# Kernel optimization log

Hardware: AMD Instinct MI355X
Metric: run time of the kernel (lower is better)

## Reference

```python
import jax, jax.numpy as jnp
import numpy as np

NEG_SLOPE = 0.2  # PyG GATv2Conv default negative_slope
EPS = 1e-16      # PyG softmax denominator eps


def _gatv2_conv(x, src, dst, Wl, bl, Wr, br, att, bias, heads, out_ch):
    """PyG GATv2Conv (share_weights=False, concat=True, self-loops already in edges)."""
    N = x.shape[0]
    xl = (x @ Wl + bl).reshape(N, heads, out_ch)  # values / source transform
    xr = (x @ Wr + br).reshape(N, heads, out_ch)  # target transform
    m = jax.nn.leaky_relu(xl[src] + xr[dst], NEG_SLOPE)      # [E,H,C]
    e = jnp.einsum('ehc,hc->eh', m, att)                      # [E,H]
    emax = jax.ops.segment_max(e, dst, num_segments=N)       # [N,H]
    ee = jnp.exp(e - emax[dst])
    denom = jax.ops.segment_sum(ee, dst, num_segments=N)
    alpha = ee / (denom[dst] + EPS)                           # scatter-softmax over dst
    out = jax.ops.segment_sum(xl[src] * alpha[:, :, None], dst, num_segments=N)
    return out.reshape(N, heads * out_ch) + bias


def setup_inputs() -> dict:
    key = jax.random.key(0)
    ks = jax.random.split(key, 16)
    N, E, DIN, DH, H, DOUT = 50000, 800000, 128, 16, 8, 64
    x = jax.random.normal(ks[0], (N, DIN), dtype=jnp.float32)
    edge_index = jax.random.randint(ks[1], (2, E), 0, N, dtype=jnp.int64)
    g = lambda k, shape: jax.random.normal(k, shape, dtype=jnp.float32) * (1.0 / np.sqrt(shape[0]))
    params = {
        'Wl1': g(ks[2], (DIN, H * DH)), 'bl1': jnp.zeros((H * DH,), jnp.float32),
        'Wr1': g(ks[3], (DIN, H * DH)), 'br1': jnp.zeros((H * DH,), jnp.float32),
        'att1': g(ks[4], (H, DH)), 'bias1': jnp.zeros((H * DH,), jnp.float32),
        'Wl2': g(ks[5], (H * DH, DOUT)), 'bl2': jnp.zeros((DOUT,), jnp.float32),
        'Wr2': g(ks[6], (H * DH, DOUT)), 'br2': jnp.zeros((DOUT,), jnp.float32),
        'att2': g(ks[7], (1, DOUT)), 'bias2': jnp.zeros((DOUT,), jnp.float32),
    }
    return {'x': x, 'edge_index': edge_index, **params}


def reference(x, edge_index, Wl1, bl1, Wr1, br1, att1, bias1,
              Wl2, bl2, Wr2, br2, att2, bias2):
    N = x.shape[0]
    loop = jnp.arange(N, dtype=edge_index.dtype)
    ei = jnp.concatenate([edge_index, jnp.stack([loop, loop])], axis=1)  # add self-loops
    src, dst = ei[0], ei[1]
    # eval mode: F.dropout is identity (p=0.6 dropouts skipped)
    h = _gatv2_conv(x, src, dst, Wl1, bl1, Wr1, br1, att1, bias1, heads=8, out_ch=16)
    h = jax.nn.elu(h)
    h = _gatv2_conv(h, src, dst, Wl2, bl2, Wr2, br2, att2, bias2, heads=1, out_ch=64)
    out = jax.nn.log_softmax(h, axis=1)
    predictions = jnp.argmax(out, axis=1)
    return (h, out, predictions)
```

## Files before the change

### kernel.cpp

```cpp
#include <hip/hip_runtime.h>
#include <hip/hip_bf16.h>

typedef unsigned short u16;
typedef __attribute__((ext_vector_type(8))) short bf8v;
typedef __attribute__((ext_vector_type(4))) float f4v;

#define N_NODES 50000
#define N_EDGES 800000
#define ET (N_EDGES + N_NODES)
#define D1 128
#define D2 64
#define NEG 0.2f
#define EPSF 1e-16f
#define NTILES_PAD 3128
#define NP (NTILES_PAD * 16)

#define O_XL1    0
#define O_XR1    6400000
#define O_AH     12800000
#define O_AM     16003072
#define O_AL     19206144
#define O_B1H    22409216
#define O_B1M    22425600
#define O_B1L    22441984
#define O_B2H    22458368
#define O_B2M    22466560
#define O_B2L    22474752
#define O_WF     22482944
#define O_SRC    22483968
#define O_DST    22908968
#define O_DEG    23333968
#define O_ROWPTR 23383968
#define O_CURSOR 23433969
#define O_CSR    23483969
#define O_FLAGS  23908969
#define O_PART   23908971

#define W_BL1   0
#define W_BR1   128
#define W_ATT1  256
#define W_BIAS1 384
#define W_BL2   512
#define W_BR2   576
#define W_ATT2  640
#define W_BIAS2 704

#define NB_SCAN  196
#define NB_CVT   3321
#define NB_PACKX 25024
#define NB_PREP1 (NB_CVT + NB_PACKX + 128 + 64 + 1)
#define NB_G1    3128
#define NB_G1S   (NB_G1 + NB_CVT)

__device__ __forceinline__ float load_f32(const void* src, int i, int isbf16) {
    if (isbf16) {
        u16 u = ((const u16*)src)[i];
        return __uint_as_float((unsigned)u << 16);
    }
    return ((const float*)src)[i];
}
__device__ __forceinline__ u16 f2b(float v) {
    __hip_bfloat16 h = __float2bfloat16(v);
    return *(u16*)&h;
}
__device__ __forceinline__ float b2f(u16 u) { return __uint_as_float((unsigned)u << 16); }

__device__ __forceinline__ void split3(float v, u16& hi, u16& mid, u16& lo) {
    hi = f2b(v);
    float r1 = v - b2f(hi);
    mid = f2b(r1);
    float r2 = r1 - b2f(mid);
    lo = f2b(r2);
}

__global__ void init_k(int* deg, const u16* x16, const int* ei32, int* flags) {
    int b = blockIdx.x;
    if (b < NB_SCAN) {
        int i = b * 256 + threadIdx.x;
        if (i < N_NODES) deg[i] = 0;
        return;
    }
    int lane = threadIdx.x;
    if (lane >= 64) return;
    int hits = 0;
    for (int j = lane; j < 32768; j += 64) {
        u16 u = x16[2 * j];
        if (((u >> 7) & 0xFF) == 0xFF) hits++;
    }
#pragma unroll
    for (int off = 32; off > 0; off >>= 1) hits += __shfl_xor(hits, off);
    int nz = 0;
    if (lane < 32) nz = ei32[2 * lane + 1];
#pragma unroll
    for (int off = 32; off > 0; off >>= 1) nz |= __shfl_xor(nz, off);
    if (lane == 0) { flags[0] = hits ? 0 : 1; flags[1] = nz ? 0 : 1; }
}

__global__ void prep1_k(const int* __restrict__ ei, u16* __restrict__ srcA, u16* __restrict__ dstA,
                        int* __restrict__ deg,
                        const void* x, u16* AH, u16* AM, u16* AL,
                        const void* Wl1, const void* Wr1, u16* B1H, u16* B1M, u16* B1L,
                        const void* Wl2, const void* Wr2, u16* B2H, u16* B2M, u16* B2L,
                        const void* bl1, const void* br1, const void* att1, const void* bias1,
                        const void* bl2, const void* br2, const void* att2, const void* bias2,
                        float* Wf, const int* flags) {
    int b = blockIdx.x, t = threadIdx.x;
    int fb = flags[0];
    if (b < NB_CVT) {
        int e = b * 256 + t;
        if (e < ET) {
            int s, d;
            if (e < N_EDGES) {
                if (flags[1]) { s = ei[2 * e]; d = ei[2 * (N_EDGES + e)]; }
                else          { s = ei[e];     d = ei[N_EDGES + e]; }
            } else {
                s = d = e - N_EDGES;
            }
            srcA[e] = (u16)s; dstA[e] = (u16)d;
            atomicAdd(&deg[d], 1);
        }
        return;
    }
    b -= NB_CVT;
    if (b < NB_PACKX) {
        int i = b * 256 + t;
        int r = i >> 7, k = i & 127;
        u16 hi = 0, mid = 0, lo = 0;
        if (r < N_NODES) split3(load_f32(x, r * D1 + k, fb), hi, mid, lo);
        int idx = (r >> 4) * 2048 + (k >> 3) * 128 + (r & 15) * 8 + (k & 7);
        AH[idx] = hi; AM[idx] = mid; AL[idx] = lo;
        return;
    }
    b -= NB_PACKX;
    if (b < 128) {
        int i = b * 256 + t;
        int k = i >> 8, n = i & 255;
        float v = (n < 128) ? load_f32(Wl1, k * 128 + n, fb)
                            : load_f32(Wr1, k * 128 + (n - 128), fb);
        u16 hi, mid, lo; split3(v, hi, mid, lo);
        int idx = ((k >> 3) * 256 + n) * 8 + (k & 7);
        B1H[idx] = hi; B1M[idx] = mid; B1L[idx] = lo;
        return;
    }
    b -= 128;
    if (b < 64) {
        int i = b * 256 + t;
        int k = i >> 7, n = i & 127;
        float v = (n < 64) ? load_f32(Wl2, k * 64 + n, fb)
                           : load_f32(Wr2, k * 64 + (n - 64), fb);
        u16 hi, mid, lo; split3(v, hi, mid, lo);
        int idx = ((k >> 3) * 128 + n) * 8 + (k & 7);
        B2H[idx] = hi; B2M[idx] = mid; B2L[idx] = lo;
        return;
    }
    if (t < 128) {
        Wf[W_BL1 + t]   = load_f32(bl1, t, fb);
        Wf[W_BR1 + t]   = load_f32(br1, t, fb);
        Wf[W_ATT1 + t]  = load_f32(att1, t, fb);
        Wf[W_BIAS1 + t] = load_f32(bias1, t, fb);
        if (t < 64) {
            Wf[W_BL2 + t]   = load_f32(bl2, t, fb);
            Wf[W_BR2 + t]   = load_f32(br2, t, fb);
            Wf[W_ATT2 + t]  = load_f32(att2, t, fb);
            Wf[W_BIAS2 + t] = load_f32(bias2, t, fb);
        }
    }
}

__global__ __launch_bounds__(256) void scanA_k(const int* __restrict__ deg, int* __restrict__ part) {
    __shared__ int s[256];
    int t = threadIdx.x, i = blockIdx.x * 256 + t;
    s[t] = (i < N_NODES) ? deg[i] : 0;
    __syncthreads();
    for (int off = 128; off > 0; off >>= 1) {
        if (t < off) s[t] += s[t + off];
        __syncthreads();
    }
    if (t == 0) part[blockIdx.x] = s[0];
}

__global__ __launch_bounds__(256) void scanB_k(int* __restrict__ part) {
    __shared__ int s[256];
    int t = threadIdx.x;
    s[t] = (t < NB_SCAN) ? part[t] : 0;
    __syncthreads();
    for (int off = 1; off < 256; off <<= 1) {
        int v = (t >= off) ? s[t - off] : 0;
        __syncthreads();
        s[t] += v;
        __syncthreads();
    }
    if (t < NB_SCAN) part[t] = (t == 0) ? 0 : s[t - 1];
}

__global__ __launch_bounds__(256) void scanC_k(const int* __restrict__ deg, const int* __restrict__ part,
                                               int* __restrict__ rowptr, int* __restrict__ cursor) {
    __shared__ int s[256];
    int t = threadIdx.x, i = blockIdx.x * 256 + t;
    int v = (i < N_NODES) ? deg[i] : 0;
    s[t] = v;
    __syncthreads();
    for (int off = 1; off < 256; off <<= 1) {
        int u = (t >= off) ? s[t - off] : 0;
        __syncthreads();
        s[t] += u;
        __syncthreads();
    }
    int excl = part[blockIdx.x] + s[t] - v;
    if (i < N_NODES) { rowptr[i] = excl; cursor[i] = excl; }
    if (i == N_NODES - 1) rowptr[N_NODES] = excl + v;
}

#define MFMA6(acc, ah, am, al, bh, bm, bl)                                    \
    acc = __builtin_amdgcn_mfma_f32_16x16x32_bf16(ah, bl, acc, 0, 0, 0);      \
    acc = __builtin_amdgcn_mfma_f32_16x16x32_bf16(am, bm, acc, 0, 0, 0);      \
    acc = __builtin_amdgcn_mfma_f32_16x16x32_bf16(al, bh, acc, 0, 0, 0);      \
    acc = __builtin_amdgcn_mfma_f32_16x16x32_bf16(ah, bm, acc, 0, 0, 0);      \
    acc = __builtin_amdgcn_mfma_f32_16x16x32_bf16(am, bh, acc, 0, 0, 0);      \
    acc = __builtin_amdgcn_mfma_f32_16x16x32_bf16(ah, bh, acc, 0, 0, 0);

__global__ __launch_bounds__(256) void g1s_k(const u16* __restrict__ AH, const u16* __restrict__ AM,
                                             const u16* __restrict__ AL,
                                             const u16* __restrict__ BH, const u16* __restrict__ BM,
                                             const u16* __restrict__ BL,
                                             const float* __restrict__ Wf,
                                             float* __restrict__ xl, float* __restrict__ xr,
                                             const u16* __restrict__ srcA, const u16* __restrict__ dstA,
                                             int* __restrict__ cursor, u16* __restrict__ csr) {
    int b = blockIdx.x;
    if (b < NB_G1) {
        int w = threadIdx.x >> 6, l = threadIdx.x & 63;
        int tile = (b >> 2) * 4 + w;
        int cb = (b & 3) << 6;
        int lr = l & 15, lg = l >> 4;
        f4v acc[4];
#pragma unroll
        for (int nt = 0; nt < 4; nt++) acc[nt] = (f4v)(0.f);
        int aoff = tile * 2048 + lg * 128 + lr * 8;
#pragma unroll
        for (int ks = 0; ks < 4; ks++) {
            bf8v ah = *(const bf8v*)(AH + aoff + ks * 512);
            bf8v am = *(const bf8v*)(AM + aoff + ks * 512);
            bf8v al = *(const bf8v*)(AL + aoff + ks * 512);
            int boff = ((ks * 4 + lg) * 256 + cb + lr) * 8;
#pragma unroll
            for (int nt = 0; nt < 4; nt++) {
                bf8v bh = *(const bf8v*)(BH + boff + nt * 128);
                bf8v bm = *(const bf8v*)(BM + boff + nt * 128);
                bf8v bl = *(const bf8v*)(BL + boff + nt * 128);
                MFMA6(acc[nt], ah, am, al, bh, bm, bl)
            }
        }
        int r0 = tile * 16 + lg * 4;
        if (r0 >= N_NODES) return;
#pragma unroll
        for (int nt = 0; nt < 4; nt++) {
            int col = cb + nt * 16 + lr;
            float bias = (col < D1) ? Wf[W_BL1 + col] : Wf[W_BR1 + col - D1];
            float* dst = (col < D1) ? (xl + col) : (xr + col - D1);
#pragma unroll
            for (int j = 0; j < 4; j++) {
                int row = r0 + j;
                dst[(size_t)row * D1] = acc[nt][j] + bias;
            }
        }
        return;
    }
    int e = (b - NB_G1) * 256 + threadIdx.x;
    if (e < ET) {
        int d = dstA[e];
        int idx = atomicAdd(&cursor[d], 1);
        csr[idx] = srcA[e];
    }
}

__global__ __launch_bounds__(256) void gemm2_mfma(const u16* __restrict__ AH, const u16* __restrict__ AM,
                                                  const u16* __restrict__ AL,
                                                  const u16* __restrict__ BH, const u16* __restrict__ BM,
                                                  const u16* __restrict__ BL,
                                                  const float* __restrict__ Wf,
                                                  float* __restrict__ xl2, float* __restrict__ xr2) {
    int w = threadIdx.x >> 6, l = threadIdx.x & 63;
    int tile = blockIdx.x * 4 + w;
    int cb = blockIdx.y << 6;
    int lr = l & 15, lg = l >> 4;
    f4v acc[4];
#pragma unroll
    for (int nt = 0; nt < 4; nt++) acc[nt] = (f4v)(0.f);
    int aoff = tile * 2048 + lg * 128 + lr * 8;
#pragma unroll
    for (int ks = 0; ks < 4; ks++) {
        bf8v ah = *(const bf8v*)(AH + aoff + ks * 512);
        bf8v am = *(const bf8v*)(AM + aoff + ks * 512);
        bf8v al = *(const bf8v*)(AL + aoff + ks * 512);
        int boff = ((ks * 4 + lg) * 128 + cb + lr) * 8;
#pragma unroll
        for (int nt = 0; nt < 4; nt++) {
            bf8v bh = *(const bf8v*)(BH + boff + nt * 128);
            bf8v bm = *(const bf8v*)(BM + boff + nt * 128);
            bf8v bl = *(const bf8v*)(BL + boff + nt * 128);
            MFMA6(acc[nt], ah, am, al, bh, bm, bl)
        }
    }
    int r0 = tile * 16 + lg * 4;
    if (r0 >= N_NODES) return;
#pragma unroll
    for (int nt = 0; nt < 4; nt++) {
        int col = cb + nt * 16 + lr;
        float bias = (col < D2) ? Wf[W_BL2 + col] : Wf[W_BR2 + col - D2];
        float* dst = (col < D2) ? (xl2 + col) : (xr2 + col - D2);
#pragma unroll
        for (int j = 0; j < 4; j++) {
            int row = r0 + j;
            dst[(size_t)row * D2] = acc[nt][j] + bias;
        }
    }
}

#define L1STEP(a)                                                              \
    {                                                                          \
        float m0 = a.x + xr4.x; m0 = fmaxf(m0, NEG * m0);                      \
        float m1 = a.y + xr4.y; m1 = fmaxf(m1, NEG * m1);                      \
        float m2 = a.z + xr4.z; m2 = fmaxf(m2, NEG * m2);                      \
        float m3 = a.w + xr4.w; m3 = fmaxf(m3, NEG * m3);                      \
        float p = m0 * at4.x + m1 * at4.y + m2 * at4.z + m3 * at4.w;           \
        p += __shfl_xor(p, 1);                                                 \
        p += __shfl_xor(p, 2);                                                 \
        p = fminf(fmaxf(p, -60.f), 60.f);                                      \
        float wgt = __expf(p);                                                 \
        l += wgt;                                                              \
        acc.x = fmaf(wgt, a.x, acc.x);                                         \
        acc.y = fmaf(wgt, a.y, acc.y);                                         \
        acc.z = fmaf(wgt, a.z, acc.z);                                         \
        acc.w = fmaf(wgt, a.w, acc.w);                                         \
    }

__global__ __launch_bounds__(256) void l1_agg(const int* __restrict__ rowptr, const u16* __restrict__ csr,
                                              const float* __restrict__ xl, const float* __restrict__ xr,
                                              const float* __restrict__ Wf,
                                              u16* __restrict__ A2H, u16* __restrict__ A2M, u16* __restrict__ A2L) {
    int n = (blockIdx.x * 256 + threadIdx.x) >> 5;
    int q = threadIdx.x & 31;
    const float4* xl4 = (const float4*)xl;
    float4 xr4 = ((const float4*)(xr + (size_t)n * D1))[q];
    float4 at4 = ((const float4*)(Wf + W_ATT1))[q];
    int i0 = rowptr[n], i1 = rowptr[n + 1];
    float l = 0.f;
    float4 acc = {0.f, 0.f, 0.f, 0.f};
    float4 a = xl4[(size_t)csr[i0] * 32 + q];
    for (int i = i0 + 1; i < i1; i++) {
        float4 an = xl4[(size_t)csr[i] * 32 + q];
        L1STEP(a)
        a = an;
    }
    L1STEP(a)
    float rinv = 1.f / l;
    float4 bi4 = ((const float4*)(Wf + W_BIAS1))[q];
    float v0 = acc.x * rinv + bi4.x; v0 = v0 > 0.f ? v0 : expm1f(v0);
    float v1 = acc.y * rinv + bi4.y; v1 = v1 > 0.f ? v1 : expm1f(v1);
    float v2 = acc.z * rinv + bi4.z; v2 = v2 > 0.f ? v2 : expm1f(v2);
    float v3 = acc.w * rinv + bi4.w; v3 = v3 > 0.f ? v3 : expm1f(v3);
    int base = (n >> 4) * 2048 + (q >> 1) * 128 + (n & 15) * 8 + (q & 1) * 4;
    ushort4 h4, m4, l4;
    split3(v0, h4.x, m4.x, l4.x);
    split3(v1, h4.y, m4.y, l4.y);
    split3(v2, h4.z, m4.z, l4.z);
    split3(v3, h4.w, m4.w, l4.w);
    *(ushort4*)(A2H + base) = h4;
    *(ushort4*)(A2M + base) = m4;
    *(ushort4*)(A2L + base) = l4;
}

#define L2STEP(a)                                                              \
    {                                                                          \
        float m0 = a.x + xr4.x; m0 = fmaxf(m0, NEG * m0);                      \
        float m1 = a.y + xr4.y; m1 = fmaxf(m1, NEG * m1);                      \
        float m2 = a.z + xr4.z; m2 = fmaxf(m2, NEG * m2);                      \
        float m3 = a.w + xr4.w; m3 = fmaxf(m3, NEG * m3);                      \
        float p = m0 * at4.x + m1 * at4.y + m2 * at4.z + m3 * at4.w;           \
        p += __shfl_xor(p, 1);                                                 \
        p += __shfl_xor(p, 2);                                                 \
        p += __shfl_xor(p, 4);                                                 \
        p += __shfl_xor(p, 8);                                                 \
        p = fminf(fmaxf(p, -80.f), 80.f);                                      \
        float wgt = __expf(p);                                                 \
        l += wgt;                                                              \
        acc.x = fmaf(wgt, a.x, acc.x);                                         \
        acc.y = fmaf(wgt, a.y, acc.y);                                         \
        acc.z = fmaf(wgt, a.z, acc.z);                                         \
        acc.w = fmaf(wgt, a.w, acc.w);                                         \
    }

__global__ __launch_bounds__(256) void l2_agg(const int* __restrict__ rowptr, const u16* __restrict__ csr,
                                              const float* __restrict__ xl, const float* __restrict__ xr,
                                              const float* __restrict__ Wf, float* __restrict__ out) {
    int n = (blockIdx.x * 256 + threadIdx.x) >> 4;
    int q = threadIdx.x & 15;
    const float4* xl4 = (const float4*)xl;
    float4 xr4 = ((const float4*)(xr + (size_t)n * D2))[q];
    float4 at4 = ((const float4*)(Wf + W_ATT2))[q];
    int i0 = rowptr[n], i1 = rowptr[n + 1];
    float l = 0.f;
    float4 acc = {0.f, 0.f, 0.f, 0.f};
    float4 a = xl4[(size_t)csr[i0] * 16 + q];
    for (int i = i0 + 1; i < i1; i++) {
        float4 an = xl4[(size_t)csr[i] * 16 + q];
        L2STEP(a)
        a = an;
    }
    L2STEP(a)
    float rinv = 1.f / (l + EPSF);
    float4 bi4 = ((const float4*)(Wf + W_BIAS2))[q];
    float v0 = acc.x * rinv + bi4.x;
    float v1 = acc.y * rinv + bi4.y;
    float v2 = acc.z * rinv + bi4.z;
    float v3 = acc.w * rinv + bi4.w;
    float4 hv = {v0, v1, v2, v3};
    ((float4*)(out + (size_t)n * D2))[q] = hv;
    float mx = fmaxf(fmaxf(v0, v1), fmaxf(v2, v3));
#pragma unroll
    for (int off = 1; off < 16; off <<= 1) mx = fmaxf(mx, __shfl_xor(mx, off));
    float sum = expf(v0 - mx) + expf(v1 - mx) + expf(v2 - mx) + expf(v3 - mx);
#pragma unroll
    for (int off = 1; off < 16; off <<= 1) sum += __shfl_xor(sum, off);
    float lse = mx + logf(sum);
    float4 ls = {v0 - lse, v1 - lse, v2 - lse, v3 - lse};
    ((float4*)(out + (size_t)N_NODES * D2 + (size_t)n * D2))[q] = ls;
    float bv = v0; int bi = 4 * q;
    if (v1 > bv) { bv = v1; bi = 4 * q + 1; }
    if (v2 > bv) { bv = v2; bi = 4 * q + 2; }
    if (v3 > bv) { bv = v3; bi = 4 * q + 3; }
#pragma unroll
    for (int off = 1; off < 16; off <<= 1) {
        float ov = __shfl_xor(bv, off);
        int   oi = __shfl_xor(bi, off);
        if (ov > bv || (ov == bv && oi < bi)) { bv = ov; bi = oi; }
    }
    if (q == 0) out[(size_t)2 * N_NODES * D2 + n] = (float)bi;
}

extern "C" void kernel_launch(void* const* d_in, const int* in_sizes, int n_in,
                              void* d_out, int out_size, void* d_ws, size_t ws_size,
                              hipStream_t stream) {
    const void* x  = d_in[0];
    const int*  ei = (const int*)d_in[1];

    float* ws = (float*)d_ws;
    float* xl1    = ws + O_XL1;
    float* xr1    = ws + O_XR1;
    u16*   AH     = (u16*)(ws + O_AH);
    u16*   AM     = (u16*)(ws + O_AM);
    u16*   AL     = (u16*)(ws + O_AL);
    u16*   B1H    = (u16*)(ws + O_B1H);
    u16*   B1M    = (u16*)(ws + O_B1M);
    u16*   B1L    = (u16*)(ws + O_B1L);
    u16*   B2H    = (u16*)(ws + O_B2H);
    u16*   B2M    = (u16*)(ws + O_B2M);
    u16*   B2L    = (u16*)(ws + O_B2L);
    float* Wf     = ws + O_WF;
    u16*   srcA   = (u16*)(ws + O_SRC);
    u16*   dstA   = (u16*)(ws + O_DST);
    int*   deg    = (int*)(ws + O_DEG);
    int*   rowptr = (int*)(ws + O_ROWPTR);
    int*   cursor = (int*)(ws + O_CURSOR);
    u16*   csr    = (u16*)(ws + O_CSR);
    int*   flags  = (int*)(ws + O_FLAGS);
    int*   part   = (int*)(ws + O_PART);

    float* xl2 = xl1;
    float* xr2 = xl1 + 3200000;

    init_k<<<NB_SCAN + 1, 256, 0, stream>>>(deg, (const u16*)x, ei, flags);
    prep1_k<<<NB_PREP1, 256, 0, stream>>>(ei, srcA, dstA, deg,
                                          x, AH, AM, AL,
                                          d_in[2], d_in[4], B1H, B1M, B1L,
                                          d_in[8], d_in[10], B2H, B2M, B2L,
                                          d_in[3], d_in[5], d_in[6], d_in[7],
                                          d_in[9], d_in[11], d_in[12], d_in[13],
                                          Wf, flags);
    scanA_k<<<NB_SCAN, 256, 0, stream>>>(deg, part);
    scanB_k<<<1, 256, 0, stream>>>(part);
    scanC_k<<<NB_SCAN, 256, 0, stream>>>(deg, part, rowptr, cursor);

    g1s_k<<<NB_G1S, 256, 0, stream>>>(AH, AM, AL, B1H, B1M, B1L, Wf, xl1, xr1,
                                      srcA, dstA, cursor, csr);
    l1_agg<<<6250, 256, 0, stream>>>(rowptr, csr, xl1, xr1, Wf, AH, AM, AL);
    gemm2_mfma<<<dim3(NTILES_PAD / 4, 2), 256, 0, stream>>>(AH, AM, AL, B2H, B2M, B2L, Wf, xl2, xr2);
    l2_agg<<<3125, 256, 0, stream>>>(rowptr, csr, xl2, xr2, Wf, (float*)d_out);
}
```

Baseline: 289.1 us.

## Vectorize x packing and co-schedule it with CSR scatter; split gemm1 out

Packing x into the hi/mid/lo bf16 tiled layout now has each thread handle 8 contiguous elements, with float4 loads and uint4 stores, replacing one-element-per-thread scalar accesses. The edge conversion and degree counting move to their own kernel. The x/weight packing is now fused with the CSR scatter after the scan, instead of fusing the scatter with gemm1. Gemm1 becomes a standalone 2D-grid kernel. This is meant to cut memory instructions in the pack stage, at the cost of one extra kernel launch and a different overlap pattern.

```diff
diff --git a/kernel.cpp b/kernel.cpp
--- a/kernel.cpp
+++ b/kernel.cpp
@@ -47,10 +47,8 @@
 
 #define NB_SCAN  196
 #define NB_CVT   3321
-#define NB_PACKX 25024
-#define NB_PREP1 (NB_CVT + NB_PACKX + 128 + 64 + 1)
-#define NB_G1    3128
-#define NB_G1S   (NB_G1 + NB_CVT)
+#define NB_PACKX 3128
+#define NB_PWS   (NB_CVT + NB_PACKX + 128 + 64 + 1)
 
 __device__ __forceinline__ float load_f32(const void* src, int i, int isbf16) {
     if (isbf16) {
@@ -96,75 +94,19 @@
     if (lane == 0) { flags[0] = hits ? 0 : 1; flags[1] = nz ? 0 : 1; }
 }
 
-__global__ void prep1_k(const int* __restrict__ ei, u16* __restrict__ srcA, u16* __restrict__ dstA,
-                        int* __restrict__ deg,
-                        const void* x, u16* AH, u16* AM, u16* AL,
-                        const void* Wl1, const void* Wr1, u16* B1H, u16* B1M, u16* B1L,
-                        const void* Wl2, const void* Wr2, u16* B2H, u16* B2M, u16* B2L,
-                        const void* bl1, const void* br1, const void* att1, const void* bias1,
-                        const void* bl2, const void* br2, const void* att2, const void* bias2,
-                        float* Wf, const int* flags) {
-    int b = blockIdx.x, t = threadIdx.x;
-    int fb = flags[0];
-    if (b < NB_CVT) {
-        int e = b * 256 + t;
-        if (e < ET) {
-            int s, d;
-            if (e < N_EDGES) {
-                if (flags[1]) { s = ei[2 * e]; d = ei[2 * (N_EDGES + e)]; }
-                else          { s = ei[e];     d = ei[N_EDGES + e]; }
-            } else {
-                s = d = e - N_EDGES;
-            }
-            srcA[e] = (u16)s; dstA[e] = (u16)d;
-            atomicAdd(&deg[d], 1);
-        }
-        return;
-    }
-    b -= NB_CVT;
-    if (b < NB_PACKX) {
-        int i = b * 256 + t;
-        int r = i >> 7, k = i & 127;
-        u16 hi = 0, mid = 0, lo = 0;
-        if (r < N_NODES) split3(load_f32(x, r * D1 + k, fb), hi, mid, lo);
-        int idx = (r >> 4) * 2048 + (k >> 3) * 128 + (r & 15) * 8 + (k & 7);
-        AH[idx] = hi; AM[idx] = mid; AL[idx] = lo;
-        return;
-    }
-    b -= NB_PACKX;
-    if (b < 128) {
-        int i = b * 256 + t;
-        int k = i >> 8, n = i & 255;
-        float v = (n < 128) ? load_f32(Wl1, k * 128 + n, fb)
-                            : load_f32(Wr1, k * 128 + (n - 128), fb);
-        u16 hi, mid, lo; split3(v, hi, mid, lo);
-        int idx = ((k >> 3) * 256 + n) * 8 + (k & 7);
-        B1H[idx] = hi; B1M[idx] = mid; B1L[idx] = lo;
-        return;
-    }
-    b -= 128;
-    if (b < 64) {
-        int i = b * 256 + t;
-        int k = i >> 7, n = i & 127;
-        float v = (n < 64) ? load_f32(Wl2, k * 64 + n, fb)
-                           : load_f32(Wr2, k * 64 + (n - 64), fb);
-        u16 hi, mid, lo; split3(v, hi, mid, lo);
-        int idx = ((k >> 3) * 128 + n) * 8 + (k & 7);
-        B2H[idx] = hi; B2M[idx] = mid; B2L[idx] = lo;
-        return;
-    }
-    if (t < 128) {
-        Wf[W_BL1 + t]   = load_f32(bl1, t, fb);
-        Wf[W_BR1 + t]   = load_f32(br1, t, fb);
-        Wf[W_ATT1 + t]  = load_f32(att1, t, fb);
-        Wf[W_BIAS1 + t] = load_f32(bias1, t, fb);
-        if (t < 64) {
-            Wf[W_BL2 + t]   = load_f32(bl2, t, fb);
-            Wf[W_BR2 + t]   = load_f32(br2, t, fb);
-            Wf[W_ATT2 + t]  = load_f32(att2, t, fb);
-            Wf[W_BIAS2 + t] = load_f32(bias2, t, fb);
-        }
-    }
+__global__ void cvt_k(const int* __restrict__ ei, const int* __restrict__ flags,
+                      u16* __restrict__ srcA, u16* __restrict__ dstA, int* __restrict__ deg) {
+    int e = blockIdx.x * 256 + threadIdx.x;
+    if (e >= ET) return;
+    int s, d;
+    if (e < N_EDGES) {
+        if (flags[1]) { s = ei[2 * e]; d = ei[2 * (N_EDGES + e)]; }
+        else          { s = ei[e];     d = ei[N_EDGES + e]; }
+    } else {
+        s = d = e - N_EDGES;
+    }
+    srcA[e] = (u16)s; dstA[e] = (u16)d;
+    atomicAdd(&deg[d], 1);
 }
 
 __global__ __launch_bounds__(256) void scanA_k(const int* __restrict__ deg, int* __restrict__ part) {
@@ -211,6 +153,87 @@
     if (i == N_NODES - 1) rowptr[N_NODES] = excl + v;
 }
 
+__global__ void pws_k(const u16* __restrict__ srcA, const u16* __restrict__ dstA,
+                      int* __restrict__ cursor, u16* __restrict__ csr,
+                      const void* x, u16* AH, u16* AM, u16* AL,
+                      const void* Wl1, const void* Wr1, u16* B1H, u16* B1M, u16* B1L,
+                      const void* Wl2, const void* Wr2, u16* B2H, u16* B2M, u16* B2L,
+                      const void* bl1, const void* br1, const void* att1, const void* bias1,
+                      const void* bl2, const void* br2, const void* att2, const void* bias2,
+                      float* Wf, const int* flags) {
+    int b = blockIdx.x, t = threadIdx.x;
+    int fb = flags[0];
+    if (b < NB_CVT) {
+        int e = b * 256 + t;
+        if (e < ET) {
+            int d = dstA[e];
+            int idx = atomicAdd(&cursor[d], 1);
+            csr[idx] = srcA[e];
+        }
+        return;
+    }
+    b -= NB_CVT;
+    if (b < NB_PACKX) {
+        int i = b * 256 + t;
+        int j = i * 8;
+        int tile = j >> 11;
+        int jj = j & 2047;
+        int r = tile * 16 + ((jj >> 3) & 15);
+        int k0 = (jj >> 7) * 8;
+        uint4 H = {0, 0, 0, 0}, M = {0, 0, 0, 0}, L = {0, 0, 0, 0};
+        u16* Hp = (u16*)&H; u16* Mp = (u16*)&M; u16* Lp = (u16*)&L;
+        if (r < N_NODES) {
+            if (fb) {
+                H = *(const uint4*)((const u16*)x + r * D1 + k0);
+            } else {
+                float4 xa = *(const float4*)((const float*)x + r * D1 + k0);
+                float4 xb = *(const float4*)((const float*)x + r * D1 + k0 + 4);
+                float vv[8] = {xa.x, xa.y, xa.z, xa.w, xb.x, xb.y, xb.z, xb.w};
+#pragma unroll
+                for (int e2 = 0; e2 < 8; e2++) split3(vv[e2], Hp[e2], Mp[e2], Lp[e2]);
+            }
+        }
+        *(uint4*)(AH + j) = H;
+        *(uint4*)(AM + j) = M;
+        *(uint4*)(AL + j) = L;
+        return;
+    }
+    b -= NB_PACKX;
+    if (b < 128) {
+        int i = b * 256 + t;
+        int k = i >> 8, n = i & 255;
+        float v = (n < 128) ? load_f32(Wl1, k * 128 + n, fb)
+                            : load_f32(Wr1, k * 128 + (n - 128), fb);
+        u16 hi, mid, lo; split3(v, hi, mid, lo);
+        int idx = ((k >> 3) * 256 + n) * 8 + (k & 7);
+        B1H[idx] = hi; B1M[idx] = mid; B1L[idx] = lo;
+        return;
+    }
+    b -= 128;
+    if (b < 64) {
+        int i = b * 256 + t;
+        int k = i >> 7, n = i & 127;
+        float v = (n < 64) ? load_f32(Wl2, k * 64 + n, fb)
+                           : load_f32(Wr2, k * 64 + (n - 64), fb);
+        u16 hi, mid, lo; split3(v, hi, mid, lo);
+        int idx = ((k >> 3) * 128 + n) * 8 + (k & 7);
+        B2H[idx] = hi; B2M[idx] = mid; B2L[idx] = lo;
+        return;
+    }
+    if (t < 128) {
+        Wf[W_BL1 + t]   = load_f32(bl1, t, fb);
+        Wf[W_BR1 + t]   = load_f32(br1, t, fb);
+        Wf[W_ATT1 + t]  = load_f32(att1, t, fb);
+        Wf[W_BIAS1 + t] = load_f32(bias1, t, fb);
+        if (t < 64) {
+            Wf[W_BL2 + t]   = load_f32(bl2, t, fb);
+            Wf[W_BR2 + t]   = load_f32(br2, t, fb);
+            Wf[W_ATT2 + t]  = load_f32(att2, t, fb);
+            Wf[W_BIAS2 + t] = load_f32(bias2, t, fb);
+        }
+    }
+}
+
 #define MFMA6(acc, ah, am, al, bh, bm, bl)                                    \
     acc = __builtin_amdgcn_mfma_f32_16x16x32_bf16(ah, bl, acc, 0, 0, 0);      \
     acc = __builtin_amdgcn_mfma_f32_16x16x32_bf16(am, bm, acc, 0, 0, 0);      \
@@ -219,58 +242,46 @@
     acc = __builtin_amdgcn_mfma_f32_16x16x32_bf16(am, bh, acc, 0, 0, 0);      \
     acc = __builtin_amdgcn_mfma_f32_16x16x32_bf16(ah, bh, acc, 0, 0, 0);
 
-__global__ __launch_bounds__(256) void g1s_k(const u16* __restrict__ AH, const u16* __restrict__ AM,
-                                             const u16* __restrict__ AL,
-                                             const u16* __restrict__ BH, const u16* __restrict__ BM,
-                                             const u16* __restrict__ BL,
-                                             const float* __restrict__ Wf,
-                                             float* __restrict__ xl, float* __restrict__ xr,
-                                             const u16* __restrict__ srcA, const u16* __restrict__ dstA,
-                                             int* __restrict__ cursor, u16* __restrict__ csr) {
-    int b = blockIdx.x;
-    if (b < NB_G1) {
-        int w = threadIdx.x >> 6, l = threadIdx.x & 63;
-        int tile = (b >> 2) * 4 + w;
-        int cb = (b & 3) << 6;
-        int lr = l & 15, lg = l >> 4;
-        f4v acc[4];
-#pragma unroll
-        for (int nt = 0; nt < 4; nt++) acc[nt] = (f4v)(0.f);
-        int aoff = tile * 2048 + lg * 128 + lr * 8;
-#pragma unroll
-        for (int ks = 0; ks < 4; ks++) {
-            bf8v ah = *(const bf8v*)(AH + aoff + ks * 512);
-            bf8v am = *(const bf8v*)(AM + aoff + ks * 512);
-            bf8v al = *(const bf8v*)(AL + aoff + ks * 512);
-            int boff = ((ks * 4 + lg) * 256 + cb + lr) * 8;
-#pragma unroll
-            for (int nt = 0; nt < 4; nt++) {
-                bf8v bh = *(const bf8v*)(BH + boff + nt * 128);
-                bf8v bm = *(const bf8v*)(BM + boff + nt * 128);
-                bf8v bl = *(const bf8v*)(BL + boff + nt * 128);
-                MFMA6(acc[nt], ah, am, al, bh, bm, bl)
-            }
-        }
-        int r0 = tile * 16 + lg * 4;
-        if (r0 >= N_NODES) return;
+__global__ __launch_bounds__(256) void gemm1_mfma(const u16* __restrict__ AH, const u16* __restrict__ AM,
+                                                  const u16* __restrict__ AL,
+                                                  const u16* __restrict__ BH, const u16* __restrict__ BM,
+                                                  const u16* __restrict__ BL,
+                                                  const float* __restrict__ Wf,
+                                                  float* __restrict__ xl, float* __restrict__ xr) {
+    int w = threadIdx.x >> 6, l = threadIdx.x & 63;
+    int tile = blockIdx.x * 4 + w;
+    int cb = blockIdx.y << 6;
+    int lr = l & 15, lg = l >> 4;
+    f4v acc[4];
+#pragma unroll
+    for (int nt = 0; nt < 4; nt++) acc[nt] = (f4v)(0.f);
+    int aoff = tile * 2048 + lg * 128 + lr * 8;
+#pragma unroll
+    for (int ks = 0; ks < 4; ks++) {
+        bf8v ah = *(const bf8v*)(AH + aoff + ks * 512);
+        bf8v am = *(const bf8v*)(AM + aoff + ks * 512);
+        bf8v al = *(const bf8v*)(AL + aoff + ks * 512);
+        int boff = ((ks * 4 + lg) * 256 + cb + lr) * 8;
 #pragma unroll
         for (int nt = 0; nt < 4; nt++) {
-            int col = cb + nt * 16 + lr;
-            float bias = (col < D1) ? Wf[W_BL1 + col] : Wf[W_BR1 + col - D1];
-            float* dst = (col < D1) ? (xl + col) : (xr + col - D1);
-#pragma unroll
-            for (int j = 0; j < 4; j++) {
-                int row = r0 + j;
-                dst[(size_t)row * D1] = acc[nt][j] + bias;
-            }
-        }
-        return;
-    }
-    int e = (b - NB_G1) * 256 + threadIdx.x;
-    if (e < ET) {
-        int d = dstA[e];
-        int idx = atomicAdd(&cursor[d], 1);
-        csr[idx] = srcA[e];
+            bf8v bh = *(const bf8v*)(BH + boff + nt * 128);
+            bf8v bm = *(const bf8v*)(BM + boff + nt * 128);
+            bf8v bl = *(const bf8v*)(BL + boff + nt * 128);
+            MFMA6(acc[nt], ah, am, al, bh, bm, bl)
+        }
+    }
+    int r0 = tile * 16 + lg * 4;
+    if (r0 >= N_NODES) return;
+#pragma unroll
+    for (int nt = 0; nt < 4; nt++) {
+        int col = cb + nt * 16 + lr;
+        float bias = (col < D1) ? Wf[W_BL1 + col] : Wf[W_BR1 + col - D1];
+        float* dst = (col < D1) ? (xl + col) : (xr + col - D1);
+#pragma unroll
+        for (int j = 0; j < 4; j++) {
+            int row = r0 + j;
+            dst[(size_t)row * D1] = acc[nt][j] + bias;
+        }
     }
 }
 
@@ -471,19 +482,19 @@
     float* xr2 = xl1 + 3200000;
 
     init_k<<<NB_SCAN + 1, 256, 0, stream>>>(deg, (const u16*)x, ei, flags);
-    prep1_k<<<NB_PREP1, 256, 0, stream>>>(ei, srcA, dstA, deg,
-                                          x, AH, AM, AL,
-                                          d_in[2], d_in[4], B1H, B1M, B1L,
-                                          d_in[8], d_in[10], B2H, B2M, B2L,
-                                          d_in[3], d_in[5], d_in[6], d_in[7],
-                                          d_in[9], d_in[11], d_in[12], d_in[13],
-                                          Wf, flags);
+    cvt_k<<<NB_CVT, 256, 0, stream>>>(ei, flags, srcA, dstA, deg);
     scanA_k<<<NB_SCAN, 256, 0, stream>>>(deg, part);
     scanB_k<<<1, 256, 0, stream>>>(part);
     scanC_k<<<NB_SCAN, 256, 0, stream>>>(deg, part, rowptr, cursor);
-
-    g1s_k<<<NB_G1S, 256, 0, stream>>>(AH, AM, AL, B1H, B1M, B1L, Wf, xl1, xr1,
-                                      srcA, dstA, cursor, csr);
+    pws_k<<<NB_PWS, 256, 0, stream>>>(srcA, dstA, cursor, csr,
+                                      x, AH, AM, AL,
+                                      d_in[2], d_in[4], B1H, B1M, B1L,
+                                      d_in[8], d_in[10], B2H, B2M, B2L,
+                                      d_in[3], d_in[5], d_in[6], d_in[7],
+                                      d_in[9], d_in[11], d_in[12], d_in[13],
+                                      Wf, flags);
+
+    gemm1_mfma<<<dim3(NTILES_PAD / 4, 4), 256, 0, stream>>>(AH, AM, AL, B1H, B1M, B1L, Wf, xl1, xr1);
     l1_agg<<<6250, 256, 0, stream>>>(rowptr, csr, xl1, xr1, Wf, AH, AM, AL);
     gemm2_mfma<<<dim3(NTILES_PAD / 4, 2), 256, 0, stream>>>(AH, AM, AL, B2H, B2M, B2L, Wf, xl2, xr2);
     l2_agg<<<3125, 256, 0, stream>>>(rowptr, csr, xl2, xr2, Wf, (float*)d_out);
```

Result: no change. 286.2 us (-1.0%).
